# Kernel optimization log

Hardware: AMD Instinct MI355X
Metric: run time of the kernel (lower is better)

The kernel has to match this reference:

```python
import jax, jax.numpy as jnp
import numpy as np

B, N, D, H, DH = 128, 128, 64, 8, 64
CBS = SBS = 4
NSEL, WIN = 2, 2
NB = N // CBS
NEG = -1e30


def _ln(x, g, b, eps=1e-5):
    mu = jnp.mean(x, -1, keepdims=True)
    var = jnp.mean((x - mu) ** 2, -1, keepdims=True)
    return (x - mu) * jax.lax.rsqrt(var + eps) * g + b


def _rms(x, g, eps=1e-6):
    return x * jax.lax.rsqrt(jnp.mean(x * x, -1, keepdims=True) + eps) * g


def _gelu(x):
    return jax.nn.gelu(x, approximate=False)


def setup_inputs() -> dict:
    key = jax.random.key(0)
    ks = iter(jax.random.split(key, 40))
    def rn(shape, s=0.05):
        return jax.random.normal(next(ks), shape, jnp.float32) * s
    return dict(
        x=jax.random.normal(next(ks), (B, N), jnp.float32),
        W_emb=rn((D,)), b_emb=rn((D,)),
        rms_scale=jnp.ones((D,), jnp.float32),
        Wq=rn((D, H * DH)), Wk=rn((D, H * DH)), Wv=rn((D, H * DH)),
        k_pos=rn((H, CBS, DH)), v_pos=rn((H, CBS, DH)),
        Wck=rn((CBS * DH, DH)), bck=rn((DH,)), Wcv=rn((CBS * DH, DH)), bcv=rn((DH,)),
        mem_ck=rn((H, 1, DH)), mem_cv=rn((H, 1, DH)),
        Wg=rn((D, 3 * H)), bg=rn((3 * H,)),
        Wo=rn((H * DH, D)),
        ln1_g=jnp.ones((D,), jnp.float32), ln1_b=jnp.zeros((D,), jnp.float32),
        Wt1=rn((N, 256)), bt1=rn((256,)), Wt2=rn((256, N)), bt2=rn((N,)),
        ln2_g=jnp.ones((D,), jnp.float32), ln2_b=jnp.zeros((D,), jnp.float32),
        Wc1=rn((D, 256)), bc1=rn((256,)), Wc2=rn((256, D)), bc2=rn((D,)),
        Wh1=rn((D, 32)), bh1=rn((32,)), Wh2=rn((32, 1)), bh2=rn((1,)),
    )


def reference(x, W_emb, b_emb, rms_scale, Wq, Wk, Wv, k_pos, v_pos, Wck, bck, Wcv, bcv,
              mem_ck, mem_cv, Wg, bg, Wo, ln1_g, ln1_b, Wt1, bt1, Wt2, bt2,
              ln2_g, ln2_b, Wc1, bc1, Wc2, bc2, Wh1, bh1, Wh2, bh2):
    scale = DH ** -0.5
    pos = jnp.arange(N)
    e = x[..., None] * W_emb + b_emb                         # [B,N,D] per-feature embedding (Linear(1,D))
    # ---- NSA sparse attention branch ----
    h = _rms(e, rms_scale)
    q = (h @ Wq).reshape(B, N, H, DH).transpose(0, 2, 1, 3)  # bhnd
    k = (h @ Wk).reshape(B, N, H, DH).transpose(0, 2, 1, 3)
    v = (h @ Wv).reshape(B, N, H, DH).transpose(0, 2, 1, 3)
    # compressed-block branch: intra-block pos emb + linear compression, 1 learned mem KV
    kb = k.reshape(B, H, NB, CBS, DH) + k_pos[None, :, None]
    vb = v.reshape(B, H, NB, CBS, DH) + v_pos[None, :, None]
    ck = kb.reshape(B, H, NB, CBS * DH) @ Wck + bck          # [B,H,NB,DH]
    cv = vb.reshape(B, H, NB, CBS * DH) @ Wcv + bcv
    ckm = jnp.concatenate([jnp.broadcast_to(mem_ck[None], (B, H, 1, DH)), ck], axis=2)
    cvm = jnp.concatenate([jnp.broadcast_to(mem_cv[None], (B, H, 1, DH)), cv], axis=2)
    cs = jnp.einsum('bhnd,bhjd->bhnj', q, ckm) * scale
    blk_end = (jnp.arange(NB) + 1) * CBS - 1                 # block fully in the past is visible
    cmask = jnp.concatenate([jnp.ones((N, 1), bool), pos[:, None] >= blk_end[None, :]], axis=1)
    cs = jnp.where(cmask[None, None], cs, NEG)
    out_c = jnp.einsum('bhnj,bhjd->bhnd', jax.nn.softmax(cs, -1), cvm)
    # fine branch: top-k selected blocks (by compressed scores) + forced causal diagonal block
    vals, sel = jax.lax.top_k(cs[..., 1:], NSEL)             # [B,H,N,NSEL]
    qblk = pos // SBS
    sel_ok = (vals > NEG / 2) & (sel != qblk[None, None, :, None])
    sel_tok = (sel[..., None] * SBS + jnp.arange(SBS)).reshape(B, H, N, NSEL * SBS)
    gather = jax.vmap(jax.vmap(lambda t, i: t[i]))           # per (b,h) token gather
    fk_sel = gather(k, sel_tok)
    fv_sel = gather(v, sel_tok)
    diag = qblk[:, None] * SBS + jnp.arange(SBS)             # [N,SBS]
    fk = jnp.concatenate([fk_sel, k[:, :, diag]], axis=3)    # [B,H,N,(NSEL+1)*SBS,DH]
    fv = jnp.concatenate([fv_sel, v[:, :, diag]], axis=3)
    fidx = jnp.concatenate([sel_tok, jnp.broadcast_to(diag[None, None], (B, H, N, SBS))], axis=3)
    fmask = (fidx <= pos[None, None, :, None]) & jnp.concatenate(
        [jnp.repeat(sel_ok, SBS, axis=-1), jnp.ones((B, H, N, SBS), bool)], axis=3)
    fs = jnp.where(fmask, jnp.einsum('bhnd,bhnsd->bhns', q, fk) * scale, NEG)
    out_f = jnp.einsum('bhns,bhnsd->bhnd', jax.nn.softmax(fs, -1), fv)
    offs = pos[:, None] - jnp.arange(WIN - 1, -1, -1)[None, :]
    oc = jnp.clip(offs, 0, None)
    wk = k[:, :, oc]
    wv = v[:, :, oc]
    ws = jnp.where((offs >= 0)[None, None], jnp.einsum('bhnd,bhnwd->bhnw', q, wk) * scale, NEG)
    out_w = jnp.einsum('bhnw,bhnwd->bhnd', jax.nn.softmax(ws, -1), wv)
    # per-head sigmoid 3-way strategy gates + output projection
    g = jax.nn.sigmoid(h @ Wg + bg).reshape(B, N, 3, H).transpose(0, 3, 2, 1)  # [B,H,3,N]
    attn = g[:, :, 0, :, None] * out_c + g[:, :, 1, :, None] * out_f + g[:, :, 2, :, None] * out_w
    x1 = attn.transpose(0, 2, 1, 3).reshape(B, N, H * DH) @ Wo
    # ---- TabMixer branch (token-mix over N, channel-mix over D) ----
    t = _ln(e, ln1_g, ln1_b).transpose(0, 2, 1)              # [B,D,N]
    m = e + (_gelu(t @ Wt1 + bt1) @ Wt2 + bt2).transpose(0, 2, 1)
    m = m + _gelu(_ln(m, ln2_g, ln2_b) @ Wc1 + bc1) @ Wc2 + bc2
    # ---- fuse, mean-pool over tokens, MLP head ----
    y = (x1 + m).mean(axis=1)
    return _gelu(y @ Wh1 + bh1) @ Wh2 + bh2                  # [B,1]
```

## Files before the change

### kernel.cpp

```cpp
#include <hip/hip_runtime.h>
#include <math.h>

#define B_ 128
#define N_ 128
#define D_ 64
#define H_ 8
#define DH_ 64
#define NEGF (-1e30f)

__device__ __forceinline__ float wred(float v) {
#pragma unroll
  for (int off = 32; off > 0; off >>= 1) v += __shfl_xor(v, off, 64);
  return v;
}

__device__ __forceinline__ float gelu_f(float x) {
  return 0.5f * x * (1.f + erff(x * 0.70710678118654752440f));
}

__global__ void k2_embed_proj(const float* __restrict__ x, const float* __restrict__ Wemb,
                              const float* __restrict__ bemb, const float* __restrict__ rmsg,
                              const float* __restrict__ ln1g, const float* __restrict__ ln1b,
                              const float* __restrict__ Wq, const float* __restrict__ Wk,
                              const float* __restrict__ Wv, const float* __restrict__ Wg,
                              const float* __restrict__ bg, float* __restrict__ e,
                              float* __restrict__ lne, float* __restrict__ q,
                              float* __restrict__ k, float* __restrict__ v,
                              float* __restrict__ g) {
  __shared__ __align__(16) float hs[32][64];
  int tid = threadIdx.x;
  int r0 = blockIdx.x * 32;
  int wave = tid >> 6, lane = tid & 63;
  for (int rr = 0; rr < 8; ++rr) {
    int r = wave * 8 + rr;
    int row = r0 + r;
    float xv = x[row];
    float ev = fmaf(xv, Wemb[lane], bemb[lane]);
    float ss = wred(ev * ev) * (1.f / 64.f);
    float hv = ev * rsqrtf(ss + 1e-6f) * rmsg[lane];
    float mu = wred(ev) * (1.f / 64.f);
    float dv = ev - mu;
    float var = wred(dv * dv) * (1.f / 64.f);
    float lv = dv * rsqrtf(var + 1e-5f) * ln1g[lane] + ln1b[lane];
    size_t o = (size_t)row * 64 + lane;
    e[o] = ev; lne[o] = lv;
    hs[r][lane] = hv;
  }
  __syncthreads();
  for (int c = tid; c < 1560; c += 256) {
    if (c < 1536) {
      int mat = c >> 9, cc = c & 511;
      const float* W = (mat == 0) ? Wq : ((mat == 1) ? Wk : Wv);
      float acc[32];
#pragma unroll
      for (int r = 0; r < 32; ++r) acc[r] = 0.f;
      for (int k4 = 0; k4 < 16; ++k4) {
        float w0 = W[(4 * k4 + 0) * 512 + cc];
        float w1 = W[(4 * k4 + 1) * 512 + cc];
        float w2 = W[(4 * k4 + 2) * 512 + cc];
        float w3 = W[(4 * k4 + 3) * 512 + cc];
#pragma unroll
        for (int r = 0; r < 32; ++r) {
          float4 hv = *(const float4*)&hs[r][4 * k4];
          acc[r] = fmaf(w0, hv.x, fmaf(w1, hv.y, fmaf(w2, hv.z, fmaf(w3, hv.w, acc[r]))));
        }
      }
      float* dst = (mat == 0) ? q : ((mat == 1) ? k : v);
      int hh = cc >> 6, d = cc & 63;
#pragma unroll
      for (int r = 0; r < 32; ++r) {
        int row = r0 + r; int bb = row >> 7, nn = row & 127;
        dst[(((size_t)bb * 8 + hh) * 128 + nn) * 64 + d] = acc[r];
      }
    } else {
      int gc = c - 1536;
      float acc[32];
#pragma unroll
      for (int r = 0; r < 32; ++r) acc[r] = 0.f;
      for (int k4 = 0; k4 < 16; ++k4) {
        float w0 = Wg[(4 * k4 + 0) * 24 + gc];
        float w1 = Wg[(4 * k4 + 1) * 24 + gc];
        float w2 = Wg[(4 * k4 + 2) * 24 + gc];
        float w3 = Wg[(4 * k4 + 3) * 24 + gc];
#pragma unroll
        for (int r = 0; r < 32; ++r) {
          float4 hv = *(const float4*)&hs[r][4 * k4];
          acc[r] = fmaf(w0, hv.x, fmaf(w1, hv.y, fmaf(w2, hv.z, fmaf(w3, hv.w, acc[r]))));
        }
      }
#pragma unroll
      for (int r = 0; r < 32; ++r)
        g[(size_t)(r0 + r) * 24 + gc] = 1.f / (1.f + __expf(-(acc[r] + bg[gc])));
    }
  }
}

__global__ void k3_compress(const float* __restrict__ k, const float* __restrict__ v,
                            const float* __restrict__ kpos, const float* __restrict__ vpos,
                            const float* __restrict__ Wck, const float* __restrict__ bck,
                            const float* __restrict__ Wcv, const float* __restrict__ bcv,
                            const float* __restrict__ mck, const float* __restrict__ mcv,
                            float* __restrict__ ckm, float* __restrict__ cvm) {
  __shared__ __align__(16) float sb[8192];
  int bh = blockIdx.x; int hh = bh & 7;
  int tid = threadIdx.x;
  int d = tid & 63, nbase = (tid >> 6) * 8;
  const float4* sb4 = (const float4*)sb;
  for (int idx = tid; idx < 8192; idx += 256) {
    int tok = idx >> 6, dd = idx & 63;
    sb[idx] = k[(size_t)bh * 8192 + idx] + kpos[(hh * 4 + (tok & 3)) * 64 + dd];
  }
  __syncthreads();
  {
    float acc[8];
#pragma unroll
    for (int i = 0; i < 8; ++i) acc[i] = bck[d];
    for (int j4 = 0; j4 < 64; ++j4) {
      float w0 = Wck[(4 * j4 + 0) * 64 + d];
      float w1 = Wck[(4 * j4 + 1) * 64 + d];
      float w2 = Wck[(4 * j4 + 2) * 64 + d];
      float w3 = Wck[(4 * j4 + 3) * 64 + d];
#pragma unroll
      for (int i = 0; i < 8; ++i) {
        float4 sv = sb4[(nbase + i) * 64 + j4];
        acc[i] = fmaf(w0, sv.x, fmaf(w1, sv.y, fmaf(w2, sv.z, fmaf(w3, sv.w, acc[i]))));
      }
    }
#pragma unroll
    for (int i = 0; i < 8; ++i) ckm[((size_t)bh * 33 + nbase + i + 1) * 64 + d] = acc[i];
    if (tid < 64) ckm[(size_t)bh * 33 * 64 + tid] = mck[hh * 64 + tid];
  }
  __syncthreads();
  for (int idx = tid; idx < 8192; idx += 256) {
    int tok = idx >> 6, dd = idx & 63;
    sb[idx] = v[(size_t)bh * 8192 + idx] + vpos[(hh * 4 + (tok & 3)) * 64 + dd];
  }
  __syncthreads();
  {
    float acc[8];
#pragma unroll
    for (int i = 0; i < 8; ++i) acc[i] = bcv[d];
    for (int j4 = 0; j4 < 64; ++j4) {
      float w0 = Wcv[(4 * j4 + 0) * 64 + d];
      float w1 = Wcv[(4 * j4 + 1) * 64 + d];
      float w2 = Wcv[(4 * j4 + 2) * 64 + d];
      float w3 = Wcv[(4 * j4 + 3) * 64 + d];
#pragma unroll
      for (int i = 0; i < 8; ++i) {
        float4 sv = sb4[(nbase + i) * 64 + j4];
        acc[i] = fmaf(w0, sv.x, fmaf(w1, sv.y, fmaf(w2, sv.z, fmaf(w3, sv.w, acc[i]))));
      }
    }
#pragma unroll
    for (int i = 0; i < 8; ++i) cvm[((size_t)bh * 33 + nbase + i + 1) * 64 + d] = acc[i];
    if (tid < 64) cvm[(size_t)bh * 33 * 64 + tid] = mcv[hh * 64 + tid];
  }
}

#define KLD 68
__global__ void __launch_bounds__(128, 2) k4_attn(
    const float* __restrict__ q, const float* __restrict__ k, const float* __restrict__ v,
    const float* __restrict__ ckm, const float* __restrict__ cvm, const float* __restrict__ g,
    float* __restrict__ attn) {
  __shared__ __align__(16) float ks[128 * KLD];
  int bh = blockIdx.x; int b = bh >> 3, hh = bh & 7;
  int tid = threadIdx.x;
  for (int idx = tid; idx < 8192; idx += 128)
    ks[(idx >> 6) * KLD + (idx & 63)] = k[(size_t)bh * 8192 + idx];
  __syncthreads();
  const int n = tid;
  float4 qr[16];
  {
    const float4* q4 = (const float4*)(q + (size_t)bh * 8192 + (size_t)n * 64);
#pragma unroll
    for (int i = 0; i < 16; ++i) {
      float4 t = q4[i];
      t.x *= 0.125f; t.y *= 0.125f; t.z *= 0.125f; t.w *= 0.125f;
      qr[i] = t;
    }
  }
  auto dot = [&](const float4* __restrict__ rp) {
    float s = 0.f;
#pragma unroll
    for (int i = 0; i < 16; ++i) {
      float4 c = rp[i];
      s = fmaf(qr[i].x, c.x, s); s = fmaf(qr[i].y, c.y, s);
      s = fmaf(qr[i].z, c.z, s); s = fmaf(qr[i].w, c.w, s);
    }
    return s;
  };
  const float* ck0 = ckm + (size_t)bh * 2112;
  const int jmax = (n + 1) >> 2;
  float scc[33];
#pragma unroll
  for (int j = 0; j < 33; ++j) {
    float s = dot((const float4*)(ck0 + j * 64));
    scc[j] = (j == 0 || j <= jmax) ? s : NEGF;
  }
  int i1 = 0; float b1 = scc[1];
#pragma unroll
  for (int j = 2; j < 33; ++j) {
    if (scc[j] > b1) { b1 = scc[j]; i1 = j - 1; }
  }
  int i2 = 0; float b2 = -3.0e38f;
// ... 27 lines not shown
  float denc = 0.f;
#pragma unroll
  for (int j = 0; j < 33; ++j) { float p = __expf(scc[j] - mxc); scc[j] = p; denc += p; }
  float mxf = sf[0];
#pragma unroll
  for (int i = 1; i < 12; ++i) mxf = fmaxf(mxf, sf[i]);
  float denf = 0.f;
#pragma unroll
  for (int i = 0; i < 12; ++i) { float p = __expf(sf[i] - mxf); sf[i] = p; denf += p; }
  float mxw = fmaxf(sw0, sw1);
  float pw0 = __expf(sw0 - mxw), pw1 = __expf(sw1 - mxw);
  const float* gr = g + (size_t)(b * 128 + n) * 24;
  float gc0 = gr[hh] / denc;
  float gf0 = gr[8 + hh] / denf;
  float gw0 = gr[16 + hh] / (pw0 + pw1);
  float4 oa[16];
#pragma unroll
  for (int i = 0; i < 16; ++i) oa[i] = make_float4(0.f, 0.f, 0.f, 0.f);
  const float* cv0 = cvm + (size_t)bh * 2112;
#pragma unroll
  for (int j = 0; j < 33; ++j) {
    float p = scc[j] * gc0;
    const float4* cr = (const float4*)(cv0 + j * 64);
#pragma unroll
    for (int i = 0; i < 16; ++i) {
      float4 c = cr[i];
      oa[i].x = fmaf(p, c.x, oa[i].x); oa[i].y = fmaf(p, c.y, oa[i].y);
      oa[i].z = fmaf(p, c.z, oa[i].z); oa[i].w = fmaf(p, c.w, oa[i].w);
    }
  }
#pragma unroll
  for (int si = 0; si < 12; ++si) {
    int tok = ((si < 4) ? row1 : (si < 8) ? row2 : rowd) + (si & 3);
    float p = sf[si] * gf0;
    const float4* vr = (const float4*)(ks + tok * KLD);
#pragma unroll
    for (int i = 0; i < 16; ++i) {
      float4 c = vr[i];
      oa[i].x = fmaf(p, c.x, oa[i].x); oa[i].y = fmaf(p, c.y, oa[i].y);
      oa[i].z = fmaf(p, c.z, oa[i].z); oa[i].w = fmaf(p, c.w, oa[i].w);
    }
  }
  {
    int nm1 = (n >= 1) ? (n - 1) : 0;
    float p0 = pw0 * gw0, p1 = pw1 * gw0;
    const float4* v0 = (const float4*)(ks + nm1 * KLD);
    const float4* v1 = (const float4*)(ks + n * KLD);
#pragma unroll
    for (int i = 0; i < 16; ++i) {
      float4 c0 = v0[i], c1 = v1[i];
      oa[i].x = fmaf(p0, c0.x, fmaf(p1, c1.x, oa[i].x));
      oa[i].y = fmaf(p0, c0.y, fmaf(p1, c1.y, oa[i].y));
      oa[i].z = fmaf(p0, c0.z, fmaf(p1, c1.z, oa[i].z));
      oa[i].w = fmaf(p0, c0.w, fmaf(p1, c1.w, oa[i].w));
    }
  }
  float4* arow = (float4*)(attn + ((size_t)(b * 128 + n)) * 512 + hh * 64);
#pragma unroll
  for (int i = 0; i < 16; ++i) arow[i] = oa[i];
}

__global__ void k5_wo(const float* __restrict__ attn, const float* __restrict__ Wo,
                      float* __restrict__ x1) {
  __shared__ __align__(16) float as[8192];
  int tid = threadIdx.x;
  size_t base = (size_t)blockIdx.x * 8192;
  for (int idx = tid; idx < 8192; idx += 256) as[idx] = attn[base + idx];
  __syncthreads();
  int d = tid & 63, rb = tid >> 6;
  const float4* as4 = (const float4*)as;
  float acc[4] = {0.f, 0.f, 0.f, 0.f};
  for (int j4 = 0; j4 < 128; ++j4) {
    float w0 = Wo[(4 * j4 + 0) * 64 + d];
    float w1 = Wo[(4 * j4 + 1) * 64 + d];
    float w2 = Wo[(4 * j4 + 2) * 64 + d];
    float w3 = Wo[(4 * j4 + 3) * 64 + d];
#pragma unroll
    for (int i = 0; i < 4; ++i) {
      float4 a = as4[(rb * 4 + i) * 128 + j4];
      acc[i] = fmaf(a.x, w0, fmaf(a.y, w1, fmaf(a.z, w2, fmaf(a.w, w3, acc[i]))));
    }
  }
  size_t r0 = (size_t)blockIdx.x * 16;
#pragma unroll
  for (int i = 0; i < 4; ++i) x1[(r0 + rb * 4 + i) * 64 + d] = acc[i];
}

__global__ void k6_token(const float* __restrict__ lne, const float* __restrict__ e,
                         const float* __restrict__ Wt1, const float* __restrict__ bt1,
                         const float* __restrict__ Wt2, const float* __restrict__ bt2,
                         float* __restrict__ m) {
  __shared__ __align__(16) float trow[8][128];
  __shared__ __align__(16) float hid[8][256];
  int b = blockIdx.x >> 3, d0 = (blockIdx.x & 7) * 8;
  int tid = threadIdx.x;
  for (int idx = tid; idx < 1024; idx += 256) {
    int nn = idx >> 3, dl = idx & 7;
    trow[dl][nn] = lne[((size_t)b * 128 + nn) * 64 + d0 + dl];
  }
  __syncthreads();
  {
    float acc[8];
#pragma unroll
    for (int i = 0; i < 8; ++i) acc[i] = 0.f;
    for (int n4 = 0; n4 < 32; ++n4) {
      float w0 = Wt1[(4 * n4 + 0) * 256 + tid];
      float w1 = Wt1[(4 * n4 + 1) * 256 + tid];
      float w2 = Wt1[(4 * n4 + 2) * 256 + tid];
      float w3 = Wt1[(4 * n4 + 3) * 256 + tid];
#pragma unroll
      for (int i = 0; i < 8; ++i) {
        float4 t = *(const float4*)&trow[i][4 * n4];
        acc[i] = fmaf(w0, t.x, fmaf(w1, t.y, fmaf(w2, t.z, fmaf(w3, t.w, acc[i]))));
      }
    }
    float bb = bt1[tid];
#pragma unroll
    for (int i = 0; i < 8; ++i) hid[i][tid] = gelu_f(acc[i] + bb);
  }
  __syncthreads();
  for (int idx = tid; idx < 1024; idx += 256) {
    int nn = idx & 127, dl = idx >> 7;
    float o = bt2[nn];
    for (int j4 = 0; j4 < 64; ++j4) {
      float4 hv = *(const float4*)&hid[dl][4 * j4];
      o = fmaf(hv.x, Wt2[(4 * j4 + 0) * 128 + nn],
          fmaf(hv.y, Wt2[(4 * j4 + 1) * 128 + nn],
          fmaf(hv.z, Wt2[(4 * j4 + 2) * 128 + nn],
          fmaf(hv.w, Wt2[(4 * j4 + 3) * 128 + nn], o))));
    }
    size_t oi = ((size_t)b * 128 + nn) * 64 + d0 + dl;
    m[oi] = e[oi] + o;
  }
}

__global__ void k7_channel(float* __restrict__ m, const float* __restrict__ g2,
                           const float* __restrict__ b2, const float* __restrict__ Wc1,
                           const float* __restrict__ bc1, const float* __restrict__ Wc2,
                           const float* __restrict__ bc2) {
  __shared__ __align__(16) float lnr[16][64];
  __shared__ __align__(16) float hid[16][256];
  int tid = threadIdx.x;
  int wv = tid >> 6, lane = tid & 63;
  size_t r0 = (size_t)blockIdx.x * 16;
  for (int rr = 0; rr < 4; ++rr) {
    int r = wv * 4 + rr;
    float mv = m[(r0 + r) * 64 + lane];
    float mu = wred(mv) * (1.f / 64.f);
    float dv = mv - mu;
    float var = wred(dv * dv) * (1.f / 64.f);
    lnr[r][lane] = dv * rsqrtf(var + 1e-5f) * g2[lane] + b2[lane];
  }
  __syncthreads();
  {
    float acc[16];
#pragma unroll
    for (int r = 0; r < 16; ++r) acc[r] = 0.f;
    for (int k4 = 0; k4 < 16; ++k4) {
      float w0 = Wc1[(4 * k4 + 0) * 256 + tid];
      float w1 = Wc1[(4 * k4 + 1) * 256 + tid];
      float w2 = Wc1[(4 * k4 + 2) * 256 + tid];
      float w3 = Wc1[(4 * k4 + 3) * 256 + tid];
#pragma unroll
      for (int r = 0; r < 16; ++r) {
        float4 t = *(const float4*)&lnr[r][4 * k4];
        acc[r] = fmaf(w0, t.x, fmaf(w1, t.y, fmaf(w2, t.z, fmaf(w3, t.w, acc[r]))));
      }
    }
    float bb = bc1[tid];
#pragma unroll
    for (int r = 0; r < 16; ++r) hid[r][tid] = gelu_f(acc[r] + bb);
  }
  __syncthreads();
  {
    float acc[4];
#pragma unroll
    for (int i = 0; i < 4; ++i) acc[i] = bc2[lane];
    for (int j4 = 0; j4 < 64; ++j4) {
      float w0 = Wc2[(4 * j4 + 0) * 64 + lane];
      float w1 = Wc2[(4 * j4 + 1) * 64 + lane];
      float w2 = Wc2[(4 * j4 + 2) * 64 + lane];
      float w3 = Wc2[(4 * j4 + 3) * 64 + lane];
#pragma unroll
      for (int i = 0; i < 4; ++i) {
        float4 t = *(const float4*)&hid[wv * 4 + i][4 * j4];
        acc[i] = fmaf(w0, t.x, fmaf(w1, t.y, fmaf(w2, t.z, fmaf(w3, t.w, acc[i]))));
      }
    }
#pragma unroll
    for (int i = 0; i < 4; ++i) {
      size_t oi = (r0 + wv * 4 + i) * 64 + lane;
      m[oi] = m[oi] + acc[i];
    }
  }
}

__global__ void k8_head(const float* __restrict__ x1, const float* __restrict__ m,
                        const float* __restrict__ Wh1, const float* __restrict__ bh1,
                        const float* __restrict__ Wh2, const float* __restrict__ bh2,
                        float* __restrict__ out) {
  __shared__ float ys[64];
  int b = blockIdx.x, lane = threadIdx.x;
  float acc = 0.f;
  for (int nn = 0; nn < 128; ++nn) {
    size_t oi = ((size_t)b * 128 + nn) * 64 + lane;
    acc += x1[oi] + m[oi];
  }
  ys[lane] = acc * (1.f / 128.f);
  __syncthreads();
  float partial = 0.f;
  if (lane < 32) {
    float a = bh1[lane];
    for (int dd = 0; dd < 64; ++dd) a = fmaf(ys[dd], Wh1[dd * 32 + lane], a);
    partial = gelu_f(a) * Wh2[lane];
  }
  partial = wred(partial);
  if (lane == 0) out[b] = partial + bh2[0];
}

extern "C" void kernel_launch(void* const* d_in, const int* in_sizes, int n_in,
                              void* d_out, int out_size, void* d_ws, size_t ws_size,
                              hipStream_t stream) {
  const float* x     = (const float*)d_in[0];
  const float* Wemb  = (const float*)d_in[1];
  const float* bemb  = (const float*)d_in[2];
  const float* rmsg  = (const float*)d_in[3];
  const float* Wq    = (const float*)d_in[4];
  const float* Wk    = (const float*)d_in[5];
  const float* Wv    = (const float*)d_in[6];
  const float* kpos  = (const float*)d_in[7];
  const float* vpos  = (const float*)d_in[8];
  const float* Wck   = (const float*)d_in[9];
// ... 25 lines not shown
  float* ws = (float*)d_ws;
  const size_t SZ_ROWD = (size_t)B_ * N_ * D_;
  const size_t SZ_BHND = (size_t)B_ * H_ * N_ * DH_;
  float* e    = ws;
  float* lne  = e + SZ_ROWD;
  float* q    = lne + SZ_ROWD;
  float* k    = q + SZ_BHND;
  float* v    = k + SZ_BHND;
  float* g    = v + SZ_BHND;
  float* ckm  = g + (size_t)B_ * N_ * 24;
  float* cvm  = ckm + (size_t)B_ * H_ * 33 * 64;
  float* attn = cvm + (size_t)B_ * H_ * 33 * 64;
  float* x1   = k;
  float* m    = v;

  k2_embed_proj<<<dim3(B_ * N_ / 32), dim3(256), 0, stream>>>(
      x, Wemb, bemb, rmsg, ln1g, ln1b, Wq, Wk, Wv, Wg, bg, e, lne, q, k, v, g);
  k3_compress<<<dim3(B_ * H_), dim3(256), 0, stream>>>(k, v, kpos, vpos, Wck, bck, Wcv, bcv, mck, mcv, ckm, cvm);
  k4_attn<<<dim3(B_ * H_), dim3(128), 0, stream>>>(q, k, v, ckm, cvm, g, attn);
  k5_wo<<<dim3(B_ * N_ / 16), dim3(256), 0, stream>>>(attn, Wo, x1);
  k6_token<<<dim3(B_ * (D_ / 8)), dim3(256), 0, stream>>>(lne, e, Wt1, bt1, Wt2, bt2, m);
  k7_channel<<<dim3(B_ * N_ / 16), dim3(256), 0, stream>>>(m, ln2g, ln2b, Wc1, bc1, Wc2, bc2);
  k8_head<<<dim3(B_), dim3(64), 0, stream>>>(x1, m, Wh1, bh1, Wh2, bh2, (float*)d_out);
}
```

Before: 499.8 us.

## Register-tile all GEMM kernels with float4 weights and split grids for parallelism

Rewrites nearly every kernel's inner matmul to use 4-wide register tiles, loading weights as float4/float2 and reading padded shared-memory rows to avoid bank conflicts. The embed/QKV projection gets a second grid dimension so each block computes one of Q, K, V plus a slice of the gate columns. The attention output accumulation is split into two halves to cut register pressure, and the dot product uses two accumulators. Token/channel mixer and head kernels are retiled with smaller row blocks and more threads so more blocks run. The projection kernel now recomputes the embedding normalisation three times, and register use may rise in the tiled loops.

```diff
diff --git a/kernel.cpp b/kernel.cpp
--- a/kernel.cpp
+++ b/kernel.cpp
@@ -18,18 +18,19 @@
   return 0.5f * x * (1.f + erff(x * 0.70710678118654752440f));
 }
 
-__global__ void k2_embed_proj(const float* __restrict__ x, const float* __restrict__ Wemb,
-                              const float* __restrict__ bemb, const float* __restrict__ rmsg,
-                              const float* __restrict__ ln1g, const float* __restrict__ ln1b,
-                              const float* __restrict__ Wq, const float* __restrict__ Wk,
-                              const float* __restrict__ Wv, const float* __restrict__ Wg,
-                              const float* __restrict__ bg, float* __restrict__ e,
-                              float* __restrict__ lne, float* __restrict__ q,
-                              float* __restrict__ k, float* __restrict__ v,
-                              float* __restrict__ g) {
-  __shared__ __align__(16) float hs[32][64];
+__global__ void __launch_bounds__(256) k2_embed_proj(
+    const float* __restrict__ x, const float* __restrict__ Wemb,
+    const float* __restrict__ bemb, const float* __restrict__ rmsg,
+    const float* __restrict__ ln1g, const float* __restrict__ ln1b,
+    const float* __restrict__ Wq, const float* __restrict__ Wk,
+    const float* __restrict__ Wv, const float* __restrict__ Wg,
+    const float* __restrict__ bg, float* __restrict__ e,
+    float* __restrict__ lne, float* __restrict__ q,
+    float* __restrict__ k, float* __restrict__ v, float* __restrict__ g) {
+  __shared__ __align__(16) float hs[32 * 68];
   int tid = threadIdx.x;
   int r0 = blockIdx.x * 32;
+  int chunk = blockIdx.y;
   int wave = tid >> 6, lane = tid & 63;
   for (int rr = 0; rr < 8; ++rr) {
     int r = wave * 8 + rr;
@@ -41,119 +42,111 @@
     float mu = wred(ev) * (1.f / 64.f);
     float dv = ev - mu;
     float var = wred(dv * dv) * (1.f / 64.f);
-    float lv = dv * rsqrtf(var + 1e-5f) * ln1g[lane] + ln1b[lane];
-    size_t o = (size_t)row * 64 + lane;
-    e[o] = ev; lne[o] = lv;
-    hs[r][lane] = hv;
-  }
-  __syncthreads();
-  for (int c = tid; c < 1560; c += 256) {
-    if (c < 1536) {
-      int mat = c >> 9, cc = c & 511;
-      const float* W = (mat == 0) ? Wq : ((mat == 1) ? Wk : Wv);
-      float acc[32];
-#pragma unroll
-      for (int r = 0; r < 32; ++r) acc[r] = 0.f;
-      for (int k4 = 0; k4 < 16; ++k4) {
-        float w0 = W[(4 * k4 + 0) * 512 + cc];
-        float w1 = W[(4 * k4 + 1) * 512 + cc];
-        float w2 = W[(4 * k4 + 2) * 512 + cc];
-        float w3 = W[(4 * k4 + 3) * 512 + cc];
-#pragma unroll
-        for (int r = 0; r < 32; ++r) {
-          float4 hv = *(const float4*)&hs[r][4 * k4];
-          acc[r] = fmaf(w0, hv.x, fmaf(w1, hv.y, fmaf(w2, hv.z, fmaf(w3, hv.w, acc[r]))));
-        }
+    if (chunk == 0) {
+      float lv = dv * rsqrtf(var + 1e-5f) * ln1g[lane] + ln1b[lane];
+      size_t o = (size_t)row * 64 + lane;
+      e[o] = ev; lne[o] = lv;
+    }
+    hs[r * 68 + lane] = hv;
+  }
+  __syncthreads();
+  const float* W = (chunk == 0) ? Wq : ((chunk == 1) ? Wk : Wv);
+  float* dst = (chunk == 0) ? q : ((chunk == 1) ? k : v);
+  {
+    int tx = tid & 127, ty = tid >> 7;
+    float4 acc[16];
+#pragma unroll
+    for (int r = 0; r < 16; ++r) acc[r] = make_float4(0.f, 0.f, 0.f, 0.f);
+    const float* Wp = W + 4 * tx;
+#pragma unroll 2
+    for (int k4 = 0; k4 < 16; ++k4) {
+      float4 w0 = *(const float4*)(Wp + (size_t)(4 * k4 + 0) * 512);
+      float4 w1 = *(const float4*)(Wp + (size_t)(4 * k4 + 1) * 512);
+      float4 w2 = *(const float4*)(Wp + (size_t)(4 * k4 + 2) * 512);
+      float4 w3 = *(const float4*)(Wp + (size_t)(4 * k4 + 3) * 512);
+#pragma unroll
+      for (int r = 0; r < 16; ++r) {
+        float4 hv = *(const float4*)&hs[(ty * 16 + r) * 68 + 4 * k4];
+        acc[r].x = fmaf(hv.x, w0.x, fmaf(hv.y, w1.x, fmaf(hv.z, w2.x, fmaf(hv.w, w3.x, acc[r].x))));
+        acc[r].y = fmaf(hv.x, w0.y, fmaf(hv.y, w1.y, fmaf(hv.z, w2.y, fmaf(hv.w, w3.y, acc[r].y))));
+        acc[r].z = fmaf(hv.x, w0.z, fmaf(hv.y, w1.z, fmaf(hv.z, w2.z, fmaf(hv.w, w3.z, acc[r].z))));
+        acc[r].w = fmaf(hv.x, w0.w, fmaf(hv.y, w1.w, fmaf(hv.z, w2.w, fmaf(hv.w, w3.w, acc[r].w))));
       }
-      float* dst = (mat == 0) ? q : ((mat == 1) ? k : v);
-      int hh = cc >> 6, d = cc & 63;
-#pragma unroll
-      for (int r = 0; r < 32; ++r) {
-        int row = r0 + r; int bb = row >> 7, nn = row & 127;
-        dst[(((size_t)bb * 8 + hh) * 128 + nn) * 64 + d] = acc[r];
-      }
-    } else {
-      int gc = c - 1536;
-      float acc[32];
-#pragma unroll
-      for (int r = 0; r < 32; ++r) acc[r] = 0.f;
-      for (int k4 = 0; k4 < 16; ++k4) {
-        float w0 = Wg[(4 * k4 + 0) * 24 + gc];
-        float w1 = Wg[(4 * k4 + 1) * 24 + gc];
-        float w2 = Wg[(4 * k4 + 2) * 24 + gc];
-        float w3 = Wg[(4 * k4 + 3) * 24 + gc];
-#pragma unroll
-        for (int r = 0; r < 32; ++r) {
-          float4 hv = *(const float4*)&hs[r][4 * k4];
-          acc[r] = fmaf(w0, hv.x, fmaf(w1, hv.y, fmaf(w2, hv.z, fmaf(w3, hv.w, acc[r]))));
-        }
-      }
-#pragma unroll
-      for (int r = 0; r < 32; ++r)
-        g[(size_t)(r0 + r) * 24 + gc] = 1.f / (1.f + __expf(-(acc[r] + bg[gc])));
-    }
-  }
-}
-
-__global__ void k3_compress(const float* __restrict__ k, const float* __restrict__ v,
-                            const float* __restrict__ kpos, const float* __restrict__ vpos,
-                            const float* __restrict__ Wck, const float* __restrict__ bck,
-                            const float* __restrict__ Wcv, const float* __restrict__ bcv,
-                            const float* __restrict__ mck, const float* __restrict__ mcv,
-                            float* __restrict__ ckm, float* __restrict__ cvm) {
-  __shared__ __align__(16) float sb[8192];
+    }
+    int hh = (4 * tx) >> 6, d4 = (4 * tx) & 63;
+    int bb = r0 >> 7;
+    float* dbase = dst + ((size_t)(bb * 8 + hh) * 128) * 64 + d4;
+#pragma unroll
+    for (int r = 0; r < 16; ++r) {
+      int nn = (r0 & 127) + ty * 16 + r;
+      *(float4*)(dbase + (size_t)nn * 64) = acc[r];
+    }
+  }
+  {
+    int r = tid >> 3, gl = tid & 7;
+    int gc = chunk * 8 + gl;
+    float a = bg[gc];
+#pragma unroll 4
+    for (int k4 = 0; k4 < 16; ++k4) {
+      float4 hv = *(const float4*)&hs[r * 68 + 4 * k4];
+      a = fmaf(hv.x, Wg[(4 * k4 + 0) * 24 + gc],
+          fmaf(hv.y, Wg[(4 * k4 + 1) * 24 + gc],
+          fmaf(hv.z, Wg[(4 * k4 + 2) * 24 + gc],
+          fmaf(hv.w, Wg[(4 * k4 + 3) * 24 + gc], a))));
+    }
+    g[(size_t)(r0 + r) * 24 + gc] = 1.f / (1.f + __expf(-a));
+  }
+}
+
+__global__ void __launch_bounds__(256) k3_compress(
+    const float* __restrict__ k, const float* __restrict__ v,
+    const float* __restrict__ kpos, const float* __restrict__ vpos,
+    const float* __restrict__ Wck, const float* __restrict__ bck,
+    const float* __restrict__ Wcv, const float* __restrict__ bcv,
+    const float* __restrict__ mck, const float* __restrict__ mcv,
+    float* __restrict__ ckm, float* __restrict__ cvm) {
+  __shared__ __align__(16) float sb[32 * 260];
   int bh = blockIdx.x; int hh = bh & 7;
   int tid = threadIdx.x;
-  int d = tid & 63, nbase = (tid >> 6) * 8;
+  int tx = tid & 15, ty = tid >> 4;
   const float4* sb4 = (const float4*)sb;
-  for (int idx = tid; idx < 8192; idx += 256) {
-    int tok = idx >> 6, dd = idx & 63;
-    sb[idx] = k[(size_t)bh * 8192 + idx] + kpos[(hh * 4 + (tok & 3)) * 64 + dd];
-  }
-  __syncthreads();
-  {
-    float acc[8];
-#pragma unroll
-    for (int i = 0; i < 8; ++i) acc[i] = bck[d];
-    for (int j4 = 0; j4 < 64; ++j4) {
-      float w0 = Wck[(4 * j4 + 0) * 64 + d];
-      float w1 = Wck[(4 * j4 + 1) * 64 + d];
-      float w2 = Wck[(4 * j4 + 2) * 64 + d];
-      float w3 = Wck[(4 * j4 + 3) * 64 + d];
-#pragma unroll
-      for (int i = 0; i < 8; ++i) {
-        float4 sv = sb4[(nbase + i) * 64 + j4];
-        acc[i] = fmaf(w0, sv.x, fmaf(w1, sv.y, fmaf(w2, sv.z, fmaf(w3, sv.w, acc[i]))));
-      }
-    }
-#pragma unroll
-    for (int i = 0; i < 8; ++i) ckm[((size_t)bh * 33 + nbase + i + 1) * 64 + d] = acc[i];
-    if (tid < 64) ckm[(size_t)bh * 33 * 64 + tid] = mck[hh * 64 + tid];
-  }
-  __syncthreads();
-  for (int idx = tid; idx < 8192; idx += 256) {
-    int tok = idx >> 6, dd = idx & 63;
-    sb[idx] = v[(size_t)bh * 8192 + idx] + vpos[(hh * 4 + (tok & 3)) * 64 + dd];
-  }
-  __syncthreads();
-  {
-    float acc[8];
-#pragma unroll
-    for (int i = 0; i < 8; ++i) acc[i] = bcv[d];
-    for (int j4 = 0; j4 < 64; ++j4) {
-      float w0 = Wcv[(4 * j4 + 0) * 64 + d];
-      float w1 = Wcv[(4 * j4 + 1) * 64 + d];
-      float w2 = Wcv[(4 * j4 + 2) * 64 + d];
-      float w3 = Wcv[(4 * j4 + 3) * 64 + d];
-#pragma unroll
-      for (int i = 0; i < 8; ++i) {
-        float4 sv = sb4[(nbase + i) * 64 + j4];
-        acc[i] = fmaf(w0, sv.x, fmaf(w1, sv.y, fmaf(w2, sv.z, fmaf(w3, sv.w, acc[i]))));
-      }
-    }
-#pragma unroll
-    for (int i = 0; i < 8; ++i) cvm[((size_t)bh * 33 + nbase + i + 1) * 64 + d] = acc[i];
-    if (tid < 64) cvm[(size_t)bh * 33 * 64 + tid] = mcv[hh * 64 + tid];
+  for (int pass = 0; pass < 2; ++pass) {
+    const float* src = pass ? v : k;
+    const float* pos = pass ? vpos : kpos;
+    const float* Wc = pass ? Wcv : Wck;
+    const float* bc = pass ? bcv : bck;
+    const float* mc = pass ? mcv : mck;
+    float* out = pass ? cvm : ckm;
+    if (pass) __syncthreads();
+    for (int idx = tid; idx < 8192; idx += 256) {
+      int tok = idx >> 6, dd = idx & 63;
+      sb[(tok >> 2) * 260 + (tok & 3) * 64 + dd] =
+          src[(size_t)bh * 8192 + idx] + pos[(hh * 4 + (tok & 3)) * 64 + dd];
+    }
+    __syncthreads();
+    float4 b4 = *(const float4*)(bc + 4 * tx);
+    float4 a0 = b4, a1 = b4;
+    const float* Wp = Wc + 4 * tx;
+#pragma unroll 2
+    for (int k4 = 0; k4 < 64; ++k4) {
+      float4 w0 = *(const float4*)(Wp + (size_t)(4 * k4 + 0) * 64);
+      float4 w1 = *(const float4*)(Wp + (size_t)(4 * k4 + 1) * 64);
+      float4 w2 = *(const float4*)(Wp + (size_t)(4 * k4 + 2) * 64);
+      float4 w3 = *(const float4*)(Wp + (size_t)(4 * k4 + 3) * 64);
+      float4 s0 = sb4[ty * 65 + k4];
+      float4 s1 = sb4[(ty + 16) * 65 + k4];
+      a0.x = fmaf(s0.x, w0.x, fmaf(s0.y, w1.x, fmaf(s0.z, w2.x, fmaf(s0.w, w3.x, a0.x))));
+      a0.y = fmaf(s0.x, w0.y, fmaf(s0.y, w1.y, fmaf(s0.z, w2.y, fmaf(s0.w, w3.y, a0.y))));
+      a0.z = fmaf(s0.x, w0.z, fmaf(s0.y, w1.z, fmaf(s0.z, w2.z, fmaf(s0.w, w3.z, a0.z))));
+      a0.w = fmaf(s0.x, w0.w, fmaf(s0.y, w1.w, fmaf(s0.z, w2.w, fmaf(s0.w, w3.w, a0.w))));
+      a1.x = fmaf(s1.x, w0.x, fmaf(s1.y, w1.x, fmaf(s1.z, w2.x, fmaf(s1.w, w3.x, a1.x))));
+      a1.y = fmaf(s1.x, w0.y, fmaf(s1.y, w1.y, fmaf(s1.z, w2.y, fmaf(s1.w, w3.y, a1.y))));
+      a1.z = fmaf(s1.x, w0.z, fmaf(s1.y, w1.z, fmaf(s1.z, w2.z, fmaf(s1.w, w3.z, a1.z))));
+      a1.w = fmaf(s1.x, w0.w, fmaf(s1.y, w1.w, fmaf(s1.z, w2.w, fmaf(s1.w, w3.w, a1.w))));
+    }
+    *(float4*)(out + ((size_t)bh * 33 + ty + 1) * 64 + 4 * tx) = a0;
+    *(float4*)(out + ((size_t)bh * 33 + ty + 17) * 64 + 4 * tx) = a1;
+    if (tid < 16) *(float4*)(out + (size_t)bh * 2112 + 4 * tid) = *(const float4*)(mc + hh * 64 + 4 * tid);
   }
 }
 
@@ -180,14 +173,16 @@
     }
   }
   auto dot = [&](const float4* __restrict__ rp) {
-    float s = 0.f;
-#pragma unroll
-    for (int i = 0; i < 16; ++i) {
-      float4 c = rp[i];
-      s = fmaf(qr[i].x, c.x, s); s = fmaf(qr[i].y, c.y, s);
-      s = fmaf(qr[i].z, c.z, s); s = fmaf(qr[i].w, c.w, s);
-    }
-    return s;
+    float s0 = 0.f, s1 = 0.f;
+#pragma unroll
+    for (int i = 0; i < 16; i += 2) {
+      float4 c0 = rp[i], c1 = rp[i + 1];
+      s0 = fmaf(qr[i].x, c0.x, s0); s0 = fmaf(qr[i].y, c0.y, s0);
+      s0 = fmaf(qr[i].z, c0.z, s0); s0 = fmaf(qr[i].w, c0.w, s0);
+      s1 = fmaf(qr[i + 1].x, c1.x, s1); s1 = fmaf(qr[i + 1].y, c1.y, s1);
+      s1 = fmaf(qr[i + 1].z, c1.z, s1); s1 = fmaf(qr[i + 1].w, c1.w, s1);
+    }
+    return s0 + s1;
   };
   const float* ck0 = ckm + (size_t)bh * 2112;
   const int jmax = (n + 1) >> 2;
@@ -245,208 +240,235 @@
   float gc0 = gr[hh] / denc;
   float gf0 = gr[8 + hh] / denf;
   float gw0 = gr[16 + hh] / (pw0 + pw1);
-  float4 oa[16];
-#pragma unroll
-  for (int i = 0; i < 16; ++i) oa[i] = make_float4(0.f, 0.f, 0.f, 0.f);
+  float pww0 = pw0 * gw0, pww1 = pw1 * gw0;
+  int nm1 = (n >= 1) ? (n - 1) : 0;
   const float* cv0 = cvm + (size_t)bh * 2112;
-#pragma unroll
-  for (int j = 0; j < 33; ++j) {
-    float p = scc[j] * gc0;
-    const float4* cr = (const float4*)(cv0 + j * 64);
-#pragma unroll
-    for (int i = 0; i < 16; ++i) {
-      float4 c = cr[i];
-      oa[i].x = fmaf(p, c.x, oa[i].x); oa[i].y = fmaf(p, c.y, oa[i].y);
-      oa[i].z = fmaf(p, c.z, oa[i].z); oa[i].w = fmaf(p, c.w, oa[i].w);
-    }
-  }
-#pragma unroll
-  for (int si = 0; si < 12; ++si) {
-    int tok = ((si < 4) ? row1 : (si < 8) ? row2 : rowd) + (si & 3);
-    float p = sf[si] * gf0;
-    const float4* vr = (const float4*)(ks + tok * KLD);
-#pragma unroll
-    for (int i = 0; i < 16; ++i) {
-      float4 c = vr[i];
-      oa[i].x = fmaf(p, c.x, oa[i].x); oa[i].y = fmaf(p, c.y, oa[i].y);
-      oa[i].z = fmaf(p, c.z, oa[i].z); oa[i].w = fmaf(p, c.w, oa[i].w);
-    }
-  }
-  {
-    int nm1 = (n >= 1) ? (n - 1) : 0;
-    float p0 = pw0 * gw0, p1 = pw1 * gw0;
-    const float4* v0 = (const float4*)(ks + nm1 * KLD);
-    const float4* v1 = (const float4*)(ks + n * KLD);
-#pragma unroll
-    for (int i = 0; i < 16; ++i) {
-      float4 c0 = v0[i], c1 = v1[i];
-      oa[i].x = fmaf(p0, c0.x, fmaf(p1, c1.x, oa[i].x));
-      oa[i].y = fmaf(p0, c0.y, fmaf(p1, c1.y, oa[i].y));
-      oa[i].z = fmaf(p0, c0.z, fmaf(p1, c1.z, oa[i].z));
-      oa[i].w = fmaf(p0, c0.w, fmaf(p1, c1.w, oa[i].w));
-    }
-  }
   float4* arow = (float4*)(attn + ((size_t)(b * 128 + n)) * 512 + hh * 64);
-#pragma unroll
-  for (int i = 0; i < 16; ++i) arow[i] = oa[i];
-}
-
-__global__ void k5_wo(const float* __restrict__ attn, const float* __restrict__ Wo,
-                      float* __restrict__ x1) {
-  __shared__ __align__(16) float as[8192];
+  for (int h2 = 0; h2 < 2; ++h2) {
+    float4 oa[8];
+#pragma unroll
+    for (int i = 0; i < 8; ++i) oa[i] = make_float4(0.f, 0.f, 0.f, 0.f);
+#pragma unroll
+    for (int j = 0; j < 33; ++j) {
+      float p = scc[j] * gc0;
+      const float4* cr = (const float4*)(cv0 + j * 64) + h2 * 8;
+#pragma unroll
+      for (int i = 0; i < 8; ++i) {
+        float4 c = cr[i];
+        oa[i].x = fmaf(p, c.x, oa[i].x); oa[i].y = fmaf(p, c.y, oa[i].y);
+        oa[i].z = fmaf(p, c.z, oa[i].z); oa[i].w = fmaf(p, c.w, oa[i].w);
+      }
+    }
+#pragma unroll
+    for (int si = 0; si < 12; ++si) {
+      int tok = ((si < 4) ? row1 : (si < 8) ? row2 : rowd) + (si & 3);
+      float p = sf[si] * gf0;
+      const float4* vr = (const float4*)(ks + tok * KLD) + h2 * 8;
+#pragma unroll
+      for (int i = 0; i < 8; ++i) {
+        float4 c = vr[i];
+        oa[i].x = fmaf(p, c.x, oa[i].x); oa[i].y = fmaf(p, c.y, oa[i].y);
+        oa[i].z = fmaf(p, c.z, oa[i].z); oa[i].w = fmaf(p, c.w, oa[i].w);
+      }
+    }
+    {
+      const float4* v0 = (const float4*)(ks + nm1 * KLD) + h2 * 8;
+      const float4* v1 = (const float4*)(ks + n * KLD) + h2 * 8;
+#pragma unroll
+      for (int i = 0; i < 8; ++i) {
+        float4 c0 = v0[i], c1 = v1[i];
+        oa[i].x = fmaf(pww0, c0.x, fmaf(pww1, c1.x, oa[i].x));
+        oa[i].y = fmaf(pww0, c0.y, fmaf(pww1, c1.y, oa[i].y));
+        oa[i].z = fmaf(pww0, c0.z, fmaf(pww1, c1.z, oa[i].z));
+        oa[i].w = fmaf(pww0, c0.w, fmaf(pww1, c1.w, oa[i].w));
+      }
+    }
+#pragma unroll
+    for (int i = 0; i < 8; ++i) arow[h2 * 8 + i] = oa[i];
+  }
+}
+
+__global__ void __launch_bounds__(256) k5_wo(const float* __restrict__ attn,
+                                             const float* __restrict__ Wo,
+                                             float* __restrict__ x1) {
+  __shared__ __align__(16) float as[16 * 516];
   int tid = threadIdx.x;
   size_t base = (size_t)blockIdx.x * 8192;
-  for (int idx = tid; idx < 8192; idx += 256) as[idx] = attn[base + idx];
-  __syncthreads();
-  int d = tid & 63, rb = tid >> 6;
+  for (int idx = tid; idx < 8192; idx += 256)
+    as[(idx >> 9) * 516 + (idx & 511)] = attn[base + idx];
+  __syncthreads();
+  int tx = tid & 15, ty = tid >> 4;
   const float4* as4 = (const float4*)as;
-  float acc[4] = {0.f, 0.f, 0.f, 0.f};
-  for (int j4 = 0; j4 < 128; ++j4) {
-    float w0 = Wo[(4 * j4 + 0) * 64 + d];
-    float w1 = Wo[(4 * j4 + 1) * 64 + d];
-    float w2 = Wo[(4 * j4 + 2) * 64 + d];
-    float w3 = Wo[(4 * j4 + 3) * 64 + d];
-#pragma unroll
-    for (int i = 0; i < 4; ++i) {
-      float4 a = as4[(rb * 4 + i) * 128 + j4];
-      acc[i] = fmaf(a.x, w0, fmaf(a.y, w1, fmaf(a.z, w2, fmaf(a.w, w3, acc[i]))));
-    }
-  }
-  size_t r0 = (size_t)blockIdx.x * 16;
-#pragma unroll
-  for (int i = 0; i < 4; ++i) x1[(r0 + rb * 4 + i) * 64 + d] = acc[i];
-}
-
-__global__ void k6_token(const float* __restrict__ lne, const float* __restrict__ e,
-                         const float* __restrict__ Wt1, const float* __restrict__ bt1,
-                         const float* __restrict__ Wt2, const float* __restrict__ bt2,
-                         float* __restrict__ m) {
-  __shared__ __align__(16) float trow[8][128];
-  __shared__ __align__(16) float hid[8][256];
-  int b = blockIdx.x >> 3, d0 = (blockIdx.x & 7) * 8;
+  float4 acc = make_float4(0.f, 0.f, 0.f, 0.f);
+  const float* Wp = Wo + 4 * tx;
+#pragma unroll 4
+  for (int k4 = 0; k4 < 128; ++k4) {
+    float4 w0 = *(const float4*)(Wp + (size_t)(4 * k4 + 0) * 64);
+    float4 w1 = *(const float4*)(Wp + (size_t)(4 * k4 + 1) * 64);
+    float4 w2 = *(const float4*)(Wp + (size_t)(4 * k4 + 2) * 64);
+    float4 w3 = *(const float4*)(Wp + (size_t)(4 * k4 + 3) * 64);
+    float4 a = as4[ty * 129 + k4];
+    acc.x = fmaf(a.x, w0.x, fmaf(a.y, w1.x, fmaf(a.z, w2.x, fmaf(a.w, w3.x, acc.x))));
+    acc.y = fmaf(a.x, w0.y, fmaf(a.y, w1.y, fmaf(a.z, w2.y, fmaf(a.w, w3.y, acc.y))));
+    acc.z = fmaf(a.x, w0.z, fmaf(a.y, w1.z, fmaf(a.z, w2.z, fmaf(a.w, w3.z, acc.z))));
+    acc.w = fmaf(a.x, w0.w, fmaf(a.y, w1.w, fmaf(a.z, w2.w, fmaf(a.w, w3.w, acc.w))));
+  }
+  *(float4*)(x1 + ((size_t)blockIdx.x * 16 + ty) * 64 + 4 * tx) = acc;
+}
+
+__global__ void __launch_bounds__(256) k6_token(
+    const float* __restrict__ lne, const float* __restrict__ e,
+    const float* __restrict__ Wt1, const float* __restrict__ bt1,
+    const float* __restrict__ Wt2, const float* __restrict__ bt2,
+    float* __restrict__ m) {
+  __shared__ __align__(16) float trow[4 * 132];
+  __shared__ __align__(16) float hid[4 * 260];
+  int b = blockIdx.x >> 4, d0 = (blockIdx.x & 15) * 4;
   int tid = threadIdx.x;
-  for (int idx = tid; idx < 1024; idx += 256) {
-    int nn = idx >> 3, dl = idx & 7;
-    trow[dl][nn] = lne[((size_t)b * 128 + nn) * 64 + d0 + dl];
-  }
-  __syncthreads();
-  {
-    float acc[8];
-#pragma unroll
-    for (int i = 0; i < 8; ++i) acc[i] = 0.f;
-    for (int n4 = 0; n4 < 32; ++n4) {
-      float w0 = Wt1[(4 * n4 + 0) * 256 + tid];
-      float w1 = Wt1[(4 * n4 + 1) * 256 + tid];
-      float w2 = Wt1[(4 * n4 + 2) * 256 + tid];
-      float w3 = Wt1[(4 * n4 + 3) * 256 + tid];
-#pragma unroll
-      for (int i = 0; i < 8; ++i) {
-        float4 t = *(const float4*)&trow[i][4 * n4];
-        acc[i] = fmaf(w0, t.x, fmaf(w1, t.y, fmaf(w2, t.z, fmaf(w3, t.w, acc[i]))));
-      }
-    }
-    float bb = bt1[tid];
-#pragma unroll
-    for (int i = 0; i < 8; ++i) hid[i][tid] = gelu_f(acc[i] + bb);
-  }
-  __syncthreads();
-  for (int idx = tid; idx < 1024; idx += 256) {
-    int nn = idx & 127, dl = idx >> 7;
-    float o = bt2[nn];
-    for (int j4 = 0; j4 < 64; ++j4) {
-      float4 hv = *(const float4*)&hid[dl][4 * j4];
-      o = fmaf(hv.x, Wt2[(4 * j4 + 0) * 128 + nn],
-          fmaf(hv.y, Wt2[(4 * j4 + 1) * 128 + nn],
-          fmaf(hv.z, Wt2[(4 * j4 + 2) * 128 + nn],
-          fmaf(hv.w, Wt2[(4 * j4 + 3) * 128 + nn], o))));
-    }
-    size_t oi = ((size_t)b * 128 + nn) * 64 + d0 + dl;
-    m[oi] = e[oi] + o;
-  }
-}
-
-__global__ void k7_channel(float* __restrict__ m, const float* __restrict__ g2,
-                           const float* __restrict__ b2, const float* __restrict__ Wc1,
-                           const float* __restrict__ bc1, const float* __restrict__ Wc2,
-                           const float* __restrict__ bc2) {
-  __shared__ __align__(16) float lnr[16][64];
-  __shared__ __align__(16) float hid[16][256];
+  for (int idx = tid; idx < 512; idx += 256) {
+    int nn = idx >> 2, dl = idx & 3;
+    trow[dl * 132 + nn] = lne[((size_t)b * 128 + nn) * 64 + d0 + dl];
+  }
+  __syncthreads();
+  {
+    int tx = tid & 63, ty = tid >> 6;
+    float4 acc = *(const float4*)(bt1 + 4 * tx);
+    const float4* tr4 = (const float4*)&trow[ty * 132];
+    const float* Wp = Wt1 + 4 * tx;
+#pragma unroll 2
+    for (int k4 = 0; k4 < 32; ++k4) {
+      float4 w0 = *(const float4*)(Wp + (size_t)(4 * k4 + 0) * 256);
+      float4 w1 = *(const float4*)(Wp + (size_t)(4 * k4 + 1) * 256);
+      float4 w2 = *(const float4*)(Wp + (size_t)(4 * k4 + 2) * 256);
+      float4 w3 = *(const float4*)(Wp + (size_t)(4 * k4 + 3) * 256);
+      float4 t = tr4[k4];
+      acc.x = fmaf(t.x, w0.x, fmaf(t.y, w1.x, fmaf(t.z, w2.x, fmaf(t.w, w3.x, acc.x))));
+      acc.y = fmaf(t.x, w0.y, fmaf(t.y, w1.y, fmaf(t.z, w2.y, fmaf(t.w, w3.y, acc.y))));
+      acc.z = fmaf(t.x, w0.z, fmaf(t.y, w1.z, fmaf(t.z, w2.z, fmaf(t.w, w3.z, acc.z))));
+      acc.w = fmaf(t.x, w0.w, fmaf(t.y, w1.w, fmaf(t.z, w2.w, fmaf(t.w, w3.w, acc.w))));
+    }
+    float* hp = &hid[ty * 260 + 4 * tx];
+    hp[0] = gelu_f(acc.x); hp[1] = gelu_f(acc.y); hp[2] = gelu_f(acc.z); hp[3] = gelu_f(acc.w);
+  }
+  __syncthreads();
+  {
+    int tx = tid & 63, ty = tid >> 6;
+    float o0 = bt2[2 * tx], o1 = bt2[2 * tx + 1];
+    const float4* h4 = (const float4*)&hid[ty * 260];
+    const float* Wp = Wt2 + 2 * tx;
+#pragma unroll 2
+    for (int k4 = 0; k4 < 64; ++k4) {
+      float2 w0 = *(const float2*)(Wp + (size_t)(4 * k4 + 0) * 128);
+      float2 w1 = *(const float2*)(Wp + (size_t)(4 * k4 + 1) * 128);
+      float2 w2 = *(const float2*)(Wp + (size_t)(4 * k4 + 2) * 128);
+      float2 w3 = *(const float2*)(Wp + (size_t)(4 * k4 + 3) * 128);
+      float4 t = h4[k4];
+      o0 = fmaf(t.x, w0.x, fmaf(t.y, w1.x, fmaf(t.z, w2.x, fmaf(t.w, w3.x, o0))));
+      o1 = fmaf(t.x, w0.y, fmaf(t.y, w1.y, fmaf(t.z, w2.y, fmaf(t.w, w3.y, o1))));
+    }
+    size_t oi0 = ((size_t)b * 128 + 2 * tx) * 64 + d0 + ty;
+    size_t oi1 = oi0 + 64;
+    m[oi0] = e[oi0] + o0;
+    m[oi1] = e[oi1] + o1;
+  }
+}
+
+__global__ void __launch_bounds__(256) k7_channel(
+    float* __restrict__ m, const float* __restrict__ g2, const float* __restrict__ b2,
+    const float* __restrict__ Wc1, const float* __restrict__ bc1,
+    const float* __restrict__ Wc2, const float* __restrict__ bc2) {
+  __shared__ __align__(16) float lnr[8 * 68];
+  __shared__ __align__(16) float hid[8 * 260];
   int tid = threadIdx.x;
   int wv = tid >> 6, lane = tid & 63;
-  size_t r0 = (size_t)blockIdx.x * 16;
-  for (int rr = 0; rr < 4; ++rr) {
-    int r = wv * 4 + rr;
+  size_t r0 = (size_t)blockIdx.x * 8;
+  for (int rr = 0; rr < 2; ++rr) {
+    int r = wv * 2 + rr;
     float mv = m[(r0 + r) * 64 + lane];
     float mu = wred(mv) * (1.f / 64.f);
     float dv = mv - mu;
     float var = wred(dv * dv) * (1.f / 64.f);
-    lnr[r][lane] = dv * rsqrtf(var + 1e-5f) * g2[lane] + b2[lane];
-  }
-  __syncthreads();
-  {
-    float acc[16];
-#pragma unroll
-    for (int r = 0; r < 16; ++r) acc[r] = 0.f;
+    lnr[r * 68 + lane] = dv * rsqrtf(var + 1e-5f) * g2[lane] + b2[lane];
+  }
+  __syncthreads();
+  {
+    int tx = tid & 63, ty = tid >> 6;
+    float4 b4 = *(const float4*)(bc1 + 4 * tx);
+    float4 a0 = b4, a1 = b4;
+    const float4* l0 = (const float4*)&lnr[ty * 68];
+    const float4* l1 = (const float4*)&lnr[(ty + 4) * 68];
+    const float* Wp = Wc1 + 4 * tx;
+#pragma unroll 2
     for (int k4 = 0; k4 < 16; ++k4) {
-      float w0 = Wc1[(4 * k4 + 0) * 256 + tid];
-      float w1 = Wc1[(4 * k4 + 1) * 256 + tid];
-      float w2 = Wc1[(4 * k4 + 2) * 256 + tid];
-      float w3 = Wc1[(4 * k4 + 3) * 256 + tid];
-#pragma unroll
-      for (int r = 0; r < 16; ++r) {
-        float4 t = *(const float4*)&lnr[r][4 * k4];
-        acc[r] = fmaf(w0, t.x, fmaf(w1, t.y, fmaf(w2, t.z, fmaf(w3, t.w, acc[r]))));
-      }
-    }
-    float bb = bc1[tid];
-#pragma unroll
-    for (int r = 0; r < 16; ++r) hid[r][tid] = gelu_f(acc[r] + bb);
-  }
-  __syncthreads();
-  {
-    float acc[4];
-#pragma unroll
-    for (int i = 0; i < 4; ++i) acc[i] = bc2[lane];
-    for (int j4 = 0; j4 < 64; ++j4) {
-      float w0 = Wc2[(4 * j4 + 0) * 64 + lane];
-      float w1 = Wc2[(4 * j4 + 1) * 64 + lane];
-      float w2 = Wc2[(4 * j4 + 2) * 64 + lane];
-      float w3 = Wc2[(4 * j4 + 3) * 64 + lane];
-#pragma unroll
-      for (int i = 0; i < 4; ++i) {
-        float4 t = *(const float4*)&hid[wv * 4 + i][4 * j4];
-        acc[i] = fmaf(w0, t.x, fmaf(w1, t.y, fmaf(w2, t.z, fmaf(w3, t.w, acc[i]))));
-      }
-    }
-#pragma unroll
-    for (int i = 0; i < 4; ++i) {
-      size_t oi = (r0 + wv * 4 + i) * 64 + lane;
-      m[oi] = m[oi] + acc[i];
-    }
-  }
-}
-
-__global__ void k8_head(const float* __restrict__ x1, const float* __restrict__ m,
-                        const float* __restrict__ Wh1, const float* __restrict__ bh1,
-                        const float* __restrict__ Wh2, const float* __restrict__ bh2,
-                        float* __restrict__ out) {
+      float4 w0 = *(const float4*)(Wp + (size_t)(4 * k4 + 0) * 256);
+      float4 w1 = *(const float4*)(Wp + (size_t)(4 * k4 + 1) * 256);
+      float4 w2 = *(const float4*)(Wp + (size_t)(4 * k4 + 2) * 256);
+      float4 w3 = *(const float4*)(Wp + (size_t)(4 * k4 + 3) * 256);
+      float4 s0 = l0[k4], s1 = l1[k4];
+      a0.x = fmaf(s0.x, w0.x, fmaf(s0.y, w1.x, fmaf(s0.z, w2.x, fmaf(s0.w, w3.x, a0.x))));
+      a0.y = fmaf(s0.x, w0.y, fmaf(s0.y, w1.y, fmaf(s0.z, w2.y, fmaf(s0.w, w3.y, a0.y))));
+      a0.z = fmaf(s0.x, w0.z, fmaf(s0.y, w1.z, fmaf(s0.z, w2.z, fmaf(s0.w, w3.z, a0.z))));
+      a0.w = fmaf(s0.x, w0.w, fmaf(s0.y, w1.w, fmaf(s0.z, w2.w, fmaf(s0.w, w3.w, a0.w))));
+      a1.x = fmaf(s1.x, w0.x, fmaf(s1.y, w1.x, fmaf(s1.z, w2.x, fmaf(s1.w, w3.x, a1.x))));
+      a1.y = fmaf(s1.x, w0.y, fmaf(s1.y, w1.y, fmaf(s1.z, w2.y, fmaf(s1.w, w3.y, a1.y))));
+      a1.z = fmaf(s1.x, w0.z, fmaf(s1.y, w1.z, fmaf(s1.z, w2.z, fmaf(s1.w, w3.z, a1.z))));
+      a1.w = fmaf(s1.x, w0.w, fmaf(s1.y, w1.w, fmaf(s1.z, w2.w, fmaf(s1.w, w3.w, a1.w))));
+    }
+    float* h0 = &hid[ty * 260 + 4 * tx];
+    float* h1 = &hid[(ty + 4) * 260 + 4 * tx];
+    h0[0] = gelu_f(a0.x); h0[1] = gelu_f(a0.y); h0[2] = gelu_f(a0.z); h0[3] = gelu_f(a0.w);
+    h1[0] = gelu_f(a1.x); h1[1] = gelu_f(a1.y); h1[2] = gelu_f(a1.z); h1[3] = gelu_f(a1.w);
+  }
+  __syncthreads();
+  {
+    int tx = tid & 31, ty = tid >> 5;
+    float o0 = bc2[2 * tx], o1 = bc2[2 * tx + 1];
+    const float4* h4 = (const float4*)&hid[ty * 260];
+    const float* Wp = Wc2 + 2 * tx;
+#pragma unroll 2
+    for (int k4 = 0; k4 < 64; ++k4) {
+      float2 w0 = *(const float2*)(Wp + (size_t)(4 * k4 + 0) * 64);
+      float2 w1 = *(const float2*)(Wp + (size_t)(4 * k4 + 1) * 64);
+      float2 w2 = *(const float2*)(Wp + (size_t)(4 * k4 + 2) * 64);
+      float2 w3 = *(const float2*)(Wp + (size_t)(4 * k4 + 3) * 64);
+      float4 t = h4[k4];
+      o0 = fmaf(t.x, w0.x, fmaf(t.y, w1.x, fmaf(t.z, w2.x, fmaf(t.w, w3.x, o0))));
+      o1 = fmaf(t.x, w0.y, fmaf(t.y, w1.y, fmaf(t.z, w2.y, fmaf(t.w, w3.y, o1))));
+    }
+    size_t oi = (r0 + ty) * 64 + 2 * tx;
+    m[oi] = m[oi] + o0;
+    m[oi + 1] = m[oi + 1] + o1;
+  }
+}
+
+__global__ void __launch_bounds__(256) k8_head(
+    const float* __restrict__ x1, const float* __restrict__ m,
+    const float* __restrict__ Wh1, const float* __restrict__ bh1,
+    const float* __restrict__ Wh2, const float* __restrict__ bh2,
+    float* __restrict__ out) {
+  __shared__ float ysp[4 * 64];
   __shared__ float ys[64];
-  int b = blockIdx.x, lane = threadIdx.x;
+  int b = blockIdx.x, tid = threadIdx.x;
+  int qtr = tid >> 6, lane = tid & 63;
   float acc = 0.f;
-  for (int nn = 0; nn < 128; ++nn) {
+  for (int nn = qtr * 32; nn < qtr * 32 + 32; ++nn) {
     size_t oi = ((size_t)b * 128 + nn) * 64 + lane;
     acc += x1[oi] + m[oi];
   }
-  ys[lane] = acc * (1.f / 128.f);
-  __syncthreads();
-  float partial = 0.f;
-  if (lane < 32) {
-    float a = bh1[lane];
-    for (int dd = 0; dd < 64; ++dd) a = fmaf(ys[dd], Wh1[dd * 32 + lane], a);
-    partial = gelu_f(a) * Wh2[lane];
-  }
-  partial = wred(partial);
-  if (lane == 0) out[b] = partial + bh2[0];
+  ysp[qtr * 64 + lane] = acc;
+  __syncthreads();
+  if (tid < 64) ys[tid] = (ysp[tid] + ysp[64 + tid] + ysp[128 + tid] + ysp[192 + tid]) * (1.f / 128.f);
+  __syncthreads();
+  if (tid < 64) {
+    float partial = 0.f;
+    if (tid < 32) {
+      float a = bh1[tid];
+      for (int dd = 0; dd < 64; ++dd) a = fmaf(ys[dd], Wh1[dd * 32 + tid], a);
+      partial = gelu_f(a) * Wh2[tid];
+    }
+    partial = wred(partial);
+    if (tid == 0) out[b] = partial + bh2[0];
+  }
 }
 
 extern "C" void kernel_launch(void* const* d_in, const int* in_sizes, int n_in,
@@ -502,12 +524,12 @@
   float* x1   = k;
   float* m    = v;
 
-  k2_embed_proj<<<dim3(B_ * N_ / 32), dim3(256), 0, stream>>>(
+  k2_embed_proj<<<dim3(B_ * N_ / 32, 3), dim3(256), 0, stream>>>(
       x, Wemb, bemb, rmsg, ln1g, ln1b, Wq, Wk, Wv, Wg, bg, e, lne, q, k, v, g);
   k3_compress<<<dim3(B_ * H_), dim3(256), 0, stream>>>(k, v, kpos, vpos, Wck, bck, Wcv, bcv, mck, mcv, ckm, cvm);
   k4_attn<<<dim3(B_ * H_), dim3(128), 0, stream>>>(q, k, v, ckm, cvm, g, attn);
   k5_wo<<<dim3(B_ * N_ / 16), dim3(256), 0, stream>>>(attn, Wo, x1);
-  k6_token<<<dim3(B_ * (D_ / 8)), dim3(256), 0, stream>>>(lne, e, Wt1, bt1, Wt2, bt2, m);
-  k7_channel<<<dim3(B_ * N_ / 16), dim3(256), 0, stream>>>(m, ln2g, ln2b, Wc1, bc1, Wc2, bc2);
-  k8_head<<<dim3(B_), dim3(64), 0, stream>>>(x1, m, Wh1, bh1, Wh2, bh2, (float*)d_out);
-}
+  k6_token<<<dim3(B_ * 16), dim3(256), 0, stream>>>(lne, e, Wt1, bt1, Wt2, bt2, m);
+  k7_channel<<<dim3(B_ * N_ / 8), dim3(256), 0, stream>>>(m, ln2g, ln2b, Wc1, bc1, Wc2, bc2);
+  k8_head<<<dim3(B_), dim3(256), 0, stream>>>(x1, m, Wh1, bh1, Wh2, bh2, (float*)d_out);
+}
```

New measurement: 568.8 us. 1.14x slower.
